# Performance work log

Hardware: AMD Instinct MI355X
Metric: run time of the kernel (lower is better)

Reference implementation:

```python
import jax, jax.numpy as jnp
import numpy as np

FORGET_BIAS = 1.0

def _lstm_cell(x, h, c, W, b):
    # BasicLSTMCell: z = [x, h] @ W + b, gates in (i, j, f, o) order
    z = jnp.concatenate([x, h], axis=-1) @ W + b
    i, j, f, o = jnp.split(z, 4, axis=-1)
    c_new = c * jax.nn.sigmoid(f + FORGET_BIAS) + jax.nn.sigmoid(i) * jnp.tanh(j)
    h_new = jnp.tanh(c_new) * jax.nn.sigmoid(o)
    return h_new, c_new

def setup_inputs() -> dict:
    key = jax.random.key(0)
    k1, k2, k3, k4, k5, k6 = jax.random.split(key, 6)
    B, T, D = 256, 200, 512
    rnn_input = jax.random.normal(k1, (B, T, D), dtype=jnp.float32)
    seq_len = jax.random.randint(k2, (B,), 0, T, dtype=jnp.int32)
    s = 0.05
    W0 = jax.random.normal(k3, (2 * D, 4 * D), dtype=jnp.float32) * s
    b0 = jax.random.normal(k4, (4 * D,), dtype=jnp.float32) * s
    W1 = jax.random.normal(k5, (2 * D, 4 * D), dtype=jnp.float32) * s
    b1 = jax.random.normal(k6, (4 * D,), dtype=jnp.float32) * s
    return {"rnn_input": rnn_input, "seq_len": seq_len, "W0": W0, "b0": b0, "W1": W1, "b1": b1}

def reference(rnn_input, seq_len, W0, b0, W1, b1):
    B, T, D = rnn_input.shape
    h0 = jnp.zeros((B, D), rnn_input.dtype)
    init = (h0, h0, h0, h0)  # (h_l0, c_l0, h_l1, c_l1)

    def step(carry, inp):
        h0, c0, h1, c1 = carry
        x_t, t = inp
        # layer 0 (plain LSTM)
        h0n, c0n = _lstm_cell(x_t, h0, c0, W0, b0)
        # layer 1 (ResidualWrapper: out = cell_out + input)
        h1n, c1n = _lstm_cell(h0n, h1, c1, W1, b1)
        y = h1n + h0n
        # dynamic_rnn semantics: past seq_len, output zero and state copy-through
        valid = (t < seq_len)[:, None]
        h0n = jnp.where(valid, h0n, h0)
        c0n = jnp.where(valid, c0n, c0)
        h1n = jnp.where(valid, h1n, h1)
        c1n = jnp.where(valid, c1n, c1)
        y = jnp.where(valid, y, 0.0)
        return (h0n, c0n, h1n, c1n), y

    xs = (jnp.swapaxes(rnn_input, 0, 1), jnp.arange(T, dtype=seq_len.dtype))
    _, ys = jax.lax.scan(step, init, xs)  # ys: [T, B, D]
    return jnp.swapaxes(ys, 0, 1)  # [B, T, D]
```

## Files before the change

kernel.cpp:

```cpp
#include <hip/hip_runtime.h>

using short8 = __attribute__((ext_vector_type(8))) short;
using f32x4  = __attribute__((ext_vector_type(4))) float;
typedef unsigned short u16;
typedef unsigned int   u32;
typedef unsigned long long u64;

constexpr int Bn = 256;
constexpr int Tn = 200;
constexpr int Dn = 512;

__device__ __forceinline__ u16 f2bf(float x) {
  union { float f; unsigned u; } v; v.f = x;
  unsigned r = v.u + 0x7FFFu + ((v.u >> 16) & 1u);
  return (u16)(r >> 16);
}
__device__ __forceinline__ float sigm(float x) { return 1.0f / (1.0f + __expf(-x)); }
__device__ __forceinline__ float tanhe(float x) { return 1.0f - 2.0f / (__expf(2.0f * x) + 1.0f); }

__global__ void cvt_x_frag(const float* __restrict__ x, u16* __restrict__ xf) {
  int i = blockIdx.x * 256 + threadIdx.x;
  int lane = i & 63;
  int kkd  = (i >> 6) & 15;
  int rf   = (i >> 10) & 3;
  int mt_t = i >> 12;
  int t = mt_t % 200, mtile = mt_t / 200;
  int row = mtile * 64 + rf * 16 + (lane & 15);
  int k0  = kkd * 32 + (lane >> 4) * 8;
  const float* s = x + ((size_t)row * Tn + t) * Dn + k0;
  float4 v0 = *reinterpret_cast<const float4*>(s);
  float4 v1 = *reinterpret_cast<const float4*>(s + 4);
  short8 r;
  r[0]=(short)f2bf(v0.x); r[1]=(short)f2bf(v0.y); r[2]=(short)f2bf(v0.z); r[3]=(short)f2bf(v0.w);
  r[4]=(short)f2bf(v1.x); r[5]=(short)f2bf(v1.y); r[6]=(short)f2bf(v1.z); r[7]=(short)f2bf(v1.w);
  reinterpret_cast<short8*>(xf)[i] = r;
}

__global__ void cvt_w_frag(const float* __restrict__ W0, const float* __restrict__ W1,
                           u16* __restrict__ Wf) {
  __shared__ u16 T[64][65];
  int b = blockIdx.x;
  int nt = b & 31, kt = (b >> 5) & 15, role = b >> 9;
  const float* W = role ? W1 : W0;
  int t = threadIdx.x;
  int k0 = kt * 64, n0 = nt * 64;
  int kr = t >> 6, nl = t & 63;
#pragma unroll
  for (int r = 0; r < 16; ++r) {
    int k = r * 4 + kr;
    T[k][nl] = f2bf(W[(size_t)(k0 + k) * 2048 + n0 + nl]);
  }
  __syncthreads();
  int g = n0 >> 9;
  int dslBase = (n0 & 511) >> 4;
  int kkBase  = k0 >> 5;
  int lane = t & 63, grp = t >> 6;
  int lr = lane & 15, lk = lane >> 4;
#pragma unroll
  for (int c = grp; c < 8; c += 4) {
    int dslL = c & 3, kkL = c >> 2;
    int dsl = dslBase + dslL, kk = kkBase + kkL;
    short8 v;
#pragma unroll
    for (int e = 0; e < 8; ++e)
      v[e] = (short)T[kkL * 32 + lk * 8 + e][dslL * 16 + lr];
    *reinterpret_cast<short8*>(Wf + ((((size_t)(role * 32 + dsl) * 4 + g) * 32 + kk) * 64 + lane) * 8) = v;
  }
}

#define MFMA16 __builtin_amdgcn_mfma_f32_16x16x32_bf16
#define GLOAD_LDS(g, l) __builtin_amdgcn_global_load_lds(                    \
    (const __attribute__((address_space(1))) void*)(g),                      \
    (__attribute__((address_space(3))) void*)(l), 16, 0, 0)

#define ISS4C(A0, A1, A2, A3, P)                                             \
  asm volatile("global_load_dwordx4 %0, %4, off sc0 sc1\n\t"                 \
               "global_load_dwordx4 %1, %4, off offset:1024 sc0 sc1\n\t"     \
               "global_load_dwordx4 %2, %4, off offset:2048 sc0 sc1\n\t"     \
               "global_load_dwordx4 %3, %4, off offset:3072 sc0 sc1"         \
               : "=v"(A0), "=v"(A1), "=v"(A2), "=v"(A3) : "v"(P) : "memory")
#define ISS4N(A0, A1, A2, A3, P)                                             \
  asm volatile("global_load_dwordx4 %0, %4, off\n\t"                         \
               "global_load_dwordx4 %1, %4, off offset:1024\n\t"             \
               "global_load_dwordx4 %2, %4, off offset:2048\n\t"             \
               "global_load_dwordx4 %3, %4, off offset:3072"                 \
               : "=v"(A0), "=v"(A1), "=v"(A2), "=v"(A3) : "v"(P) : "memory")
#define WAITV(N)                                                             \
  asm volatile("s_waitcnt vmcnt(" #N ")" ::: "memory");                      \
  __builtin_amdgcn_sched_barrier(0)
#define MMK(av, kk) {                                                        \
    short8 w0 = *reinterpret_cast<const short8*>(WL + (kk) * 1024);          \
    short8 w1 = *reinterpret_cast<const short8*>(WL + 32768 + (kk) * 1024);  \
    short8 w2 = *reinterpret_cast<const short8*>(WL + 65536 + (kk) * 1024);  \
    short8 w3 = *reinterpret_cast<const short8*>(WL + 98304 + (kk) * 1024);  \
    ac0 = MFMA16(av, w0, ac0, 0, 0, 0);                                      \
    ac1 = MFMA16(av, w1, ac1, 0, 0, 0);                                      \
    ac2 = MFMA16(av, w2, ac2, 0, 0, 0);                                      \
    ac3 = MFMA16(av, w3, ac3, 0, 0, 0); }

extern "C" __global__ void __launch_bounds__(256, 1)
rnn_persist(const u16* __restrict__ xf, const u16* __restrict__ Wf,
            const float* __restrict__ b0, const float* __restrict__ b1,
            const int* __restrict__ seq,
            u16* __restrict__ hf0, u16* __restrict__ hf1,
            u32* __restrict__ bar, float* __restrict__ out) {
  extern __shared__ __align__(16) char smem[];
  const int blk = blockIdx.x;
  const int q = blk & 7;
  const int role = q & 1;
  const int mtile = q >> 1;
  const int dsl = blk >> 3;
  const int tid = threadIdx.x;
  const int rf = tid >> 6, lane = tid & 63;

  {
    const char* gsrc = reinterpret_cast<const char*>(Wf)
                     + (size_t)(role * 32 + dsl) * 131072 + tid * 16;
    char* lds = smem + tid * 16;
#pragma unroll
    for (int i = 0; i < 32; ++i)
      GLOAD_LDS(gsrc + i * 4096, lds + i * 4096);
  }

  const char* xfb = reinterpret_cast<const char*>(xf);
  const char* h0b = reinterpret_cast<const char*>(hf0);
  const char* h1b = reinterpret_cast<const char*>(hf1);
  const int aoff = rf * 16384 + lane * 16;
  const char* WL = smem + lane * 16;

  const int d0 = dsl * 16 + (lane & 15);
  const float* bias = role ? b1 : b0;
  const float bg0 = bias[d0], bg1 = bias[512 + d0], bg2 = bias[1024 + d0], bg3 = bias[1536 + d0];
  const int rowB = mtile * 64 + rf * 16 + (lane >> 4) * 4;
  int sl[4];
#pragma unroll
  for (int e = 0; e < 4; ++e) sl[e] = seq[rowB + e];

  const int kkd = dsl >> 1;
  const int lane_t_base = ((((dsl & 1) << 1) | ((lane & 15) >> 3)) << 4) + (lane >> 4) * 4;
  const size_t hoff0 = (size_t)mtile * 32768 + (size_t)(rf * 16 + kkd) * 512
                     + (size_t)lane_t_base * 8 + (lane & 7);

  u16* hfSelf = role ? hf1 : hf0;
  u16* stg = reinterpret_cast<u16*>(smem + 131072);
  const int uu = tid & 63;
  const size_t o8 = (size_t)((mtile * 4 + rf) * 16 + kkd) * 128
                  + ((dsl & 1) * 32 + (uu >> 1)) * 2 + (uu & 1);
  u32* flagme = bar + mtile * 64 + role * 32 + dsl;
  const u32* fb = bar + mtile * 64 + tid;

  float creg[4]  = {0.f, 0.f, 0.f, 0.f};
  float hkeep[4] = {0.f, 0.f, 0.f, 0.f};

  __syncthreads();

#pragma unroll 1
  for (int p = 0; p <= Tn; ++p) {
    const bool act = role ? (p >= 1) : (p < Tn);
    const int Rp = (p & 1) ^ 1, Wp = p & 1;
    if (act) {
      const int tcur = role ? (p - 1) : p;
      const size_t hRp = (size_t)Rp * 262144 + (size_t)mtile * 65536;
      const char* Alo = (role == 0)
          ? xfb + ((size_t)mtile * Tn + p) * 65536 + aoff
          : h0b + hRp + aoff;
      const char* Ahi = (role == 0) ? h0b + hRp + aoff : h1b + hRp + aoff;

      const char* hra = reinterpret_cast<const char*>(
          reinterpret_cast<const u16*>(h0b) + (size_t)Rp * 131072 + hoff0);
      u32 hn0, hn1, hn2, hn3;
      asm volatile("global_load_ushort %0, %4, off sc0 sc1\n\t"
                   "global_load_ushort %1, %4, off offset:16 sc0 sc1\n\t"
                   "global_load_ushort %2, %4, off offset:32 sc0 sc1\n\t"
                   "global_load_ushort %3, %4, off offset:48 sc0 sc1"
                   : "=v"(hn0), "=v"(hn1), "=v"(hn2), "=v"(hn3) : "v"(hra) : "memory");

      short8 A0,A1,A2,A3,A4,A5,A6,A7,A8,A9,A10,A11,A12,A13,A14,A15;
      short8 B0,B1,B2,B3,B4,B5,B6,B7,B8,B9,B10,B11,B12,B13,B14,B15;
      if (role == 0) {
        ISS4N(A0,A1,A2,A3,    Alo);
        ISS4N(A4,A5,A6,A7,    Alo + 4096);
        ISS4N(A8,A9,A10,A11,  Alo + 8192);
        ISS4N(A12,A13,A14,A15,Alo + 12288);
      } else {
        ISS4C(A0,A1,A2,A3,    Alo);
        ISS4C(A4,A5,A6,A7,    Alo + 4096);
        ISS4C(A8,A9,A10,A11,  Alo + 8192);
        ISS4C(A12,A13,A14,A15,Alo + 12288);
      }
      ISS4C(B0,B1,B2,B3,    Ahi);
      ISS4C(B4,B5,B6,B7,    Ahi + 4096);
      ISS4C(B8,B9,B10,B11,  Ahi + 8192);
      ISS4C(B12,B13,B14,B15,Ahi + 12288);

      f32x4 ac0 = {0.f,0.f,0.f,0.f}, ac1 = {0.f,0.f,0.f,0.f};
      f32x4 ac2 = {0.f,0.f,0.f,0.f}, ac3 = {0.f,0.f,0.f,0.f};

      WAITV(28); MMK(A0,0)  MMK(A1,1)  MMK(A2,2)  MMK(A3,3)
      WAITV(24); MMK(A4,4)  MMK(A5,5)  MMK(A6,6)  MMK(A7,7)
      WAITV(20); MMK(A8,8)  MMK(A9,9)  MMK(A10,10) MMK(A11,11)
      WAITV(16); MMK(A12,12) MMK(A13,13) MMK(A14,14) MMK(A15,15)
      WAITV(12); MMK(B0,16) MMK(B1,17) MMK(B2,18) MMK(B3,19)
      WAITV(8);  MMK(B4,20) MMK(B5,21) MMK(B6,22) MMK(B7,23)
      WAITV(4);  MMK(B8,24) MMK(B9,25) MMK(B10,26) MMK(B11,27)
      WAITV(0);  MMK(B12,28) MMK(B13,29) MMK(B14,30) MMK(B15,31)

      const u32 hnv[4] = {hn0, hn1, hn2, hn3};
#pragma unroll
      for (int e = 0; e < 4; ++e) {
        float zi = ac0[e] + bg0, zj = ac1[e] + bg1, zf = ac2[e] + bg2, zo = ac3[e] + bg3;
        float cprev = creg[e];
        float cn = cprev * sigm(zf + 1.0f) + sigm(zi) * tanhe(zj);
        float hn = tanhe(cn) * sigm(zo);
        bool valid = tcur < sl[e];
        float hk = valid ? hn : hkeep[e];
        creg[e] = valid ? cn : cprev;
        hkeep[e] = hk;
        stg[rf * 256 + (((lane & 15) >> 3) * 16 + (lane >> 4) * 4 + e) * 8 + (lane & 7)] = f2bf(hk);
        if (role) {
          union { float f; u32 u; } hv; hv.u = hnv[e] << 16;
          out[((size_t)(rowB + e) * Tn + tcur) * Dn + d0] = valid ? (hn + hv.f) : 0.0f;
        }
      }
      __syncthreads();
      {
        u64 v = reinterpret_cast<const u64*>(stg)[tid];
        u64* ha = reinterpret_cast<u64*>(hfSelf + (size_t)Wp * 131072) + o8;
        asm volatile("global_store_dwordx2 %0, %1, off sc0 sc1" :: "v"(ha), "v"(v) : "memory");
      }
      asm volatile("s_waitcnt vmcnt(0)" ::: "memory");
    }

    if (p == Tn) break;

    __syncthreads();
    if (tid == 0) {
      u32 tv = (u32)(p + 1);
      asm volatile("global_store_dword %0, %1, off sc0 sc1" :: "v"(flagme), "v"(tv) : "memory");
    }
    if (tid < 64) {
      const int tgt = p + 1;
      u32 fv;
      do {
        asm volatile("global_load_dword %0, %1, off sc0 sc1\n\t"
                     "s_waitcnt vmcnt(0)"
                     : "=v"(fv) : "v"(fb) : "memory");
      } while (!__all((int)fv >= tgt));
    }
    __syncthreads();
  }
}

#define LDA(kk) (*reinterpret_cast<const short8*>(                           \
    (kk) < 16 ? (Alo + (size_t)(kk) * 1024) : (Ahi + (size_t)((kk) - 16) * 1024)))

extern "C" __global__ void __launch_bounds__(256, 1)
rnn_step(const u16* __restrict__ xf, const u16* __restrict__ Wf,
         const float* __restrict__ b0, const float* __restrict__ b1,
         const int* __restrict__ seq,
         u16* __restrict__ hf0, u16* __restrict__ hf1,
         float* __restrict__ cbuf, float* __restrict__ out, int p) {
  extern __shared__ __align__(16) char smem[];
  const int blk = blockIdx.x;
  const int role = blk & 1;
  const int mtile = (blk >> 1) & 3;
  const int dsl = blk >> 3;
  const bool act = role ? (p >= 1) : (p < Tn);
  if (!act) return;

  const int tid = threadIdx.x;
  const int rf = tid >> 6, lane = tid & 63;
  const int Rp = (p & 1) ^ 1, Wp = p & 1;
  const int tcur = role ? (p - 1) : p;

  {
    const char* gsrc = reinterpret_cast<const char*>(Wf)
                     + (size_t)(role * 32 + dsl) * 131072 + tid * 16;
    char* lds = smem + tid * 16;
#pragma unroll
    for (int i = 0; i < 32; ++i)
      GLOAD_LDS(gsrc + i * 4096, lds + i * 4096);
  }

  const char* h0base = reinterpret_cast<const char*>(hf0);
  const char* h1base = reinterpret_cast<const char*>(hf1);
  const size_t hRp = (size_t)Rp * 262144 + (size_t)mtile * 65536;
  const int aoff = rf * 16384 + lane * 16;

  const char* Alo;
  const char* Ahi;
  if (role == 0) {
    Alo = reinterpret_cast<const char*>(xf) + ((size_t)mtile * Tn + p) * 65536 + aoff;
    Ahi = h0base + hRp + aoff;
  } else {
    Alo = h0base + hRp + aoff;
    Ahi = h1base + hRp + aoff;
  }
  const char* WL = smem + lane * 16;

  short8 ca0 = LDA(0), ca1 = LDA(1), ca2 = LDA(2), ca3 = LDA(3);

  const int d0 = dsl * 16 + (lane & 15);
  const float* bias = role ? b1 : b0;
  const float bg0 = bias[d0], bg1 = bias[512 + d0], bg2 = bias[1024 + d0], bg3 = bias[1536 + d0];
  const int rowB = mtile * 64 + rf * 16 + (lane >> 4) * 4;
  int sl[4];
#pragma unroll
  for (int e = 0; e < 4; ++e) sl[e] = seq[rowB + e];

  const int kkd = dsl >> 1;
  const int lane_t_base = ((((dsl & 1) << 1) | ((lane & 15) >> 3)) << 4) + (lane >> 4) * 4;
  const size_t hoff0 = (size_t)mtile * 32768 + (size_t)(rf * 16 + kkd) * 512
                     + (size_t)lane_t_base * 8 + (lane & 7);

  u16 h0nraw[4];
  if (role) {
    const u16* hr = reinterpret_cast<const u16*>(h0base) + (size_t)Rp * 131072;
#pragma unroll
    for (int e = 0; e < 4; ++e) h0nraw[e] = hr[hoff0 + e * 8];
  }
  float* cme = cbuf + ((size_t)blk * 256 + tid) * 4;
  float cpre[4];
#pragma unroll
  for (int e = 0; e < 4; ++e) cpre[e] = cme[e];
  u16* hfSelf = role ? hf1 : hf0;
  const u16* hprev = hfSelf + (size_t)Rp * 131072;
  u16 hp16[4];
#pragma unroll
  for (int e = 0; e < 4; ++e) hp16[e] = hprev[hoff0 + e * 8];

  __syncthreads();

  f32x4 ac0 = {0.f,0.f,0.f,0.f}, ac1 = {0.f,0.f,0.f,0.f};
  f32x4 ac2 = {0.f,0.f,0.f,0.f}, ac3 = {0.f,0.f,0.f,0.f};
  short8 na0, na1, na2, na3;
#pragma unroll
  for (int c = 0; c < 8; ++c) {
    const int k0 = c * 4;
    if (c < 7) {
      na0 = LDA(k0 + 4); na1 = LDA(k0 + 5); na2 = LDA(k0 + 6); na3 = LDA(k0 + 7);
    }
#pragma unroll
    for (int j = 0; j < 4; ++j) {
      const int kk = k0 + j;
      short8 a = (j == 0) ? ca0 : (j == 1) ? ca1 : (j == 2) ? ca2 : ca3;
      short8 w0 = *reinterpret_cast<const short8*>(WL + kk * 1024);
      short8 w1 = *reinterpret_cast<const short8*>(WL + 32768 + kk * 1024);
      short8 w2 = *reinterpret_cast<const short8*>(WL + 65536 + kk * 1024);
      short8 w3 = *reinterpret_cast<const short8*>(WL + 98304 + kk * 1024);
      ac0 = MFMA16(a, w0, ac0, 0, 0, 0);
      ac1 = MFMA16(a, w1, ac1, 0, 0, 0);
      ac2 = MFMA16(a, w2, ac2, 0, 0, 0);
      ac3 = MFMA16(a, w3, ac3, 0, 0, 0);
    }
    ca0 = na0; ca1 = na1; ca2 = na2; ca3 = na3;
  }

  u16* stg = reinterpret_cast<u16*>(smem + 131072);
#pragma unroll
  for (int e = 0; e < 4; ++e) {
    float zi = ac0[e] + bg0, zj = ac1[e] + bg1, zf = ac2[e] + bg2, zo = ac3[e] + bg3;
    float cprev = cpre[e];
    float cn = cprev * sigm(zf + 1.0f) + sigm(zi) * tanhe(zj);
    float hn = tanhe(cn) * sigm(zo);
    bool valid = tcur < sl[e];
    union { float f; u32 u; } hp; hp.u = ((u32)hp16[e]) << 16;
    float hkeep = valid ? hn : hp.f;
    cme[e] = valid ? cn : cprev;
    stg[rf * 256 + (((lane & 15) >> 3) * 16 + (lane >> 4) * 4 + e) * 8 + (lane & 7)] = f2bf(hkeep);
    if (role) {
      union { float f; u32 u; } hv; hv.u = ((u32)h0nraw[e]) << 16;
      out[((size_t)(rowB + e) * Tn + tcur) * Dn + d0] = valid ? (hn + hv.f) : 0.0f;
    }
  }
  __syncthreads();
  {
    const int rft = tid >> 6, u = tid & 63;
    u64 v = reinterpret_cast<const u64*>(stg)[tid];
    u64* hw8 = reinterpret_cast<u64*>(hfSelf + (size_t)Wp * 131072);
    size_t o8 = (size_t)((mtile * 4 + rft) * 16 + kkd) * 128 + ((dsl & 1) * 32 + (u >> 1)) * 2 + (u & 1);
    hw8[o8] = v;
  }
}

extern "C" void kernel_launch(void* const* d_in, const int* in_sizes, int n_in,
                              void* d_out, int out_size, void* d_ws, size_t ws_size,
                              hipStream_t stream) {
  (void)in_sizes; (void)n_in; (void)out_size; (void)ws_size;
  const float* x  = (const float*)d_in[0];
  const int* seq  = (const int*)d_in[1];
  const float* W0 = (const float*)d_in[2];
  const float* b0 = (const float*)d_in[3];
  const float* W1 = (const float*)d_in[4];
  const float* b1 = (const float*)d_in[5];
  float* out = (float*)d_out;

  char* ws = (char*)d_ws;
  u16*  xf   = (u16*)(ws);
  u16*  Wf   = (u16*)(ws + 52428800);
  u16*  hf0  = (u16*)(ws + 60817408);
  u16*  hf1  = (u16*)(ws + 61341696);
  u32*  bar  = (u32*)(ws + 61865984);
  float* cbuf = (float*)(ws + 61865984);

  hipMemsetAsync(ws + 60817408, 0, 2097152, stream);
  hipLaunchKernelGGL(cvt_x_frag, dim3(12800), dim3(256), 0, stream, x, xf);
  hipLaunchKernelGGL(cvt_w_frag, dim3(1024), dim3(256), 0, stream, W0, W1, Wf);

  hipFuncSetAttribute((const void*)rnn_persist,
                      hipFuncAttributeMaxDynamicSharedMemorySize, 133120);
  hipFuncSetAttribute((const void*)rnn_step,
                      hipFuncAttributeMaxDynamicSharedMemorySize, 133120);

  void* args[] = { (void*)&xf, (void*)&Wf, (void*)&b0, (void*)&b1, (void*)&seq,
                   (void*)&hf0, (void*)&hf1, (void*)&bar, (void*)&out };
  hipError_t err = hipLaunchCooperativeKernel((void*)rnn_persist, dim3(256), dim3(256),
                                              args, 133120, stream);
  if (err != hipSuccess) {
    for (int p = 0; p <= Tn; ++p) {
      hipLaunchKernelGGL(rnn_step, dim3(256), dim3(256), 133120, stream,
                         xf, Wf, b0, b1, seq, hf0, hf1, cbuf, out, p);
    }
  }
}
```

Before: 1.203 ms.

## Prefetch next-step x tiles and defer output stores past the barrier

Layer-0 blocks now issue the input x fragment loads for step p+1 before the inter-block barrier, so that load latency overlaps the spin-wait instead of sitting on the recurrent critical path. Layer-1 blocks buffer their outputs in registers and write them after signalling the flag, which keeps the output stores off the pre-barrier vmcnt(0) wait. Memory clobbers are dropped from the load asm and the sched_barrier mask is relaxed to give the compiler more scheduling freedom. The risks are higher register pressure from the 16 prefetch registers held live across the loop, and possible ordering hazards from removing the memory clobbers.

```diff
diff --git a/kernel.cpp b/kernel.cpp
--- a/kernel.cpp
+++ b/kernel.cpp
@@ -78,16 +78,16 @@
                "global_load_dwordx4 %1, %4, off offset:1024 sc0 sc1\n\t"     \
                "global_load_dwordx4 %2, %4, off offset:2048 sc0 sc1\n\t"     \
                "global_load_dwordx4 %3, %4, off offset:3072 sc0 sc1"         \
-               : "=v"(A0), "=v"(A1), "=v"(A2), "=v"(A3) : "v"(P) : "memory")
+               : "=v"(A0), "=v"(A1), "=v"(A2), "=v"(A3) : "v"(P))
 #define ISS4N(A0, A1, A2, A3, P)                                             \
   asm volatile("global_load_dwordx4 %0, %4, off\n\t"                         \
                "global_load_dwordx4 %1, %4, off offset:1024\n\t"             \
                "global_load_dwordx4 %2, %4, off offset:2048\n\t"             \
                "global_load_dwordx4 %3, %4, off offset:3072"                 \
-               : "=v"(A0), "=v"(A1), "=v"(A2), "=v"(A3) : "v"(P) : "memory")
+               : "=v"(A0), "=v"(A1), "=v"(A2), "=v"(A3) : "v"(P))
 #define WAITV(N)                                                             \
-  asm volatile("s_waitcnt vmcnt(" #N ")" ::: "memory");                      \
-  __builtin_amdgcn_sched_barrier(0)
+  asm volatile("s_waitcnt vmcnt(" #N ")");                                   \
+  __builtin_amdgcn_sched_barrier(0x3F7)
 #define MMK(av, kk) {                                                        \
     short8 w0 = *reinterpret_cast<const short8*>(WL + (kk) * 1024);          \
     short8 w1 = *reinterpret_cast<const short8*>(WL + 32768 + (kk) * 1024);  \
@@ -152,58 +152,74 @@
   float creg[4]  = {0.f, 0.f, 0.f, 0.f};
   float hkeep[4] = {0.f, 0.f, 0.f, 0.f};
 
+  short8 A0,A1,A2,A3,A4,A5,A6,A7,A8,A9,A10,A11,A12,A13,A14,A15;
+  short8 B0,B1,B2,B3,B4,B5,B6,B7,B8,B9,B10,B11,B12,B13,B14,B15;
+
+  if (role == 0) {
+    const char* An = xfb + ((size_t)mtile * Tn + 0) * 65536 + aoff;
+    ISS4N(A0,A1,A2,A3,    An);
+    ISS4N(A4,A5,A6,A7,    An + 4096);
+    ISS4N(A8,A9,A10,A11,  An + 8192);
+    ISS4N(A12,A13,A14,A15,An + 12288);
+  }
+
   __syncthreads();
 
 #pragma unroll 1
   for (int p = 0; p <= Tn; ++p) {
     const bool act = role ? (p >= 1) : (p < Tn);
     const int Rp = (p & 1) ^ 1, Wp = p & 1;
+    float outv[4] = {0.f, 0.f, 0.f, 0.f};
     if (act) {
       const int tcur = role ? (p - 1) : p;
       const size_t hRp = (size_t)Rp * 262144 + (size_t)mtile * 65536;
-      const char* Alo = (role == 0)
-          ? xfb + ((size_t)mtile * Tn + p) * 65536 + aoff
-          : h0b + hRp + aoff;
-      const char* Ahi = (role == 0) ? h0b + hRp + aoff : h1b + hRp + aoff;
-
-      const char* hra = reinterpret_cast<const char*>(
-          reinterpret_cast<const u16*>(h0b) + (size_t)Rp * 131072 + hoff0);
-      u32 hn0, hn1, hn2, hn3;
-      asm volatile("global_load_ushort %0, %4, off sc0 sc1\n\t"
-                   "global_load_ushort %1, %4, off offset:16 sc0 sc1\n\t"
-                   "global_load_ushort %2, %4, off offset:32 sc0 sc1\n\t"
-                   "global_load_ushort %3, %4, off offset:48 sc0 sc1"
-                   : "=v"(hn0), "=v"(hn1), "=v"(hn2), "=v"(hn3) : "v"(hra) : "memory");
-
-      short8 A0,A1,A2,A3,A4,A5,A6,A7,A8,A9,A10,A11,A12,A13,A14,A15;
-      short8 B0,B1,B2,B3,B4,B5,B6,B7,B8,B9,B10,B11,B12,B13,B14,B15;
+
+      f32x4 ac0 = {0.f,0.f,0.f,0.f}, ac1 = {0.f,0.f,0.f,0.f};
+      f32x4 ac2 = {0.f,0.f,0.f,0.f}, ac3 = {0.f,0.f,0.f,0.f};
+      u32 hn0 = 0, hn1 = 0, hn2 = 0, hn3 = 0;
+
       if (role == 0) {
-        ISS4N(A0,A1,A2,A3,    Alo);
-        ISS4N(A4,A5,A6,A7,    Alo + 4096);
-        ISS4N(A8,A9,A10,A11,  Alo + 8192);
-        ISS4N(A12,A13,A14,A15,Alo + 12288);
+        const char* Bh = h0b + hRp + aoff;
+        ISS4C(B0,B1,B2,B3,    Bh);
+        ISS4C(B4,B5,B6,B7,    Bh + 4096);
+        ISS4C(B8,B9,B10,B11,  Bh + 8192);
+        ISS4C(B12,B13,B14,B15,Bh + 12288);
+        WAITV(16);
+        MMK(A0,0)  MMK(A1,1)  MMK(A2,2)  MMK(A3,3)
+        MMK(A4,4)  MMK(A5,5)  MMK(A6,6)  MMK(A7,7)
+        MMK(A8,8)  MMK(A9,9)  MMK(A10,10) MMK(A11,11)
+        MMK(A12,12) MMK(A13,13) MMK(A14,14) MMK(A15,15)
+        WAITV(12); MMK(B0,16) MMK(B1,17) MMK(B2,18) MMK(B3,19)
+        WAITV(8);  MMK(B4,20) MMK(B5,21) MMK(B6,22) MMK(B7,23)
+        WAITV(4);  MMK(B8,24) MMK(B9,25) MMK(B10,26) MMK(B11,27)
+        WAITV(0);  MMK(B12,28) MMK(B13,29) MMK(B14,30) MMK(B15,31)
       } else {
+        const char* hra = reinterpret_cast<const char*>(
+            reinterpret_cast<const u16*>(h0b) + (size_t)Rp * 131072 + hoff0);
+        asm volatile("global_load_ushort %0, %4, off sc0 sc1\n\t"
+                     "global_load_ushort %1, %4, off offset:16 sc0 sc1\n\t"
+                     "global_load_ushort %2, %4, off offset:32 sc0 sc1\n\t"
+                     "global_load_ushort %3, %4, off offset:48 sc0 sc1"
+                     : "=v"(hn0), "=v"(hn1), "=v"(hn2), "=v"(hn3) : "v"(hra));
+        const char* Alo = h0b + hRp + aoff;
+        const char* Ahi = h1b + hRp + aoff;
         ISS4C(A0,A1,A2,A3,    Alo);
         ISS4C(A4,A5,A6,A7,    Alo + 4096);
         ISS4C(A8,A9,A10,A11,  Alo + 8192);
         ISS4C(A12,A13,A14,A15,Alo + 12288);
+        ISS4C(B0,B1,B2,B3,    Ahi);
+        ISS4C(B4,B5,B6,B7,    Ahi + 4096);
+        ISS4C(B8,B9,B10,B11,  Ahi + 8192);
+        ISS4C(B12,B13,B14,B15,Ahi + 12288);
+        WAITV(28); MMK(A0,0)  MMK(A1,1)  MMK(A2,2)  MMK(A3,3)
+        WAITV(24); MMK(A4,4)  MMK(A5,5)  MMK(A6,6)  MMK(A7,7)
+        WAITV(20); MMK(A8,8)  MMK(A9,9)  MMK(A10,10) MMK(A11,11)
+        WAITV(16); MMK(A12,12) MMK(A13,13) MMK(A14,14) MMK(A15,15)
+        WAITV(12); MMK(B0,16) MMK(B1,17) MMK(B2,18) MMK(B3,19)
+        WAITV(8);  MMK(B4,20) MMK(B5,21) MMK(B6,22) MMK(B7,23)
+        WAITV(4);  MMK(B8,24) MMK(B9,25) MMK(B10,26) MMK(B11,27)
+        WAITV(0);  MMK(B12,28) MMK(B13,29) MMK(B14,30) MMK(B15,31)
       }
-      ISS4C(B0,B1,B2,B3,    Ahi);
-      ISS4C(B4,B5,B6,B7,    Ahi + 4096);
-      ISS4C(B8,B9,B10,B11,  Ahi + 8192);
-      ISS4C(B12,B13,B14,B15,Ahi + 12288);
-
-      f32x4 ac0 = {0.f,0.f,0.f,0.f}, ac1 = {0.f,0.f,0.f,0.f};
-      f32x4 ac2 = {0.f,0.f,0.f,0.f}, ac3 = {0.f,0.f,0.f,0.f};
-
-      WAITV(28); MMK(A0,0)  MMK(A1,1)  MMK(A2,2)  MMK(A3,3)
-      WAITV(24); MMK(A4,4)  MMK(A5,5)  MMK(A6,6)  MMK(A7,7)
-      WAITV(20); MMK(A8,8)  MMK(A9,9)  MMK(A10,10) MMK(A11,11)
-      WAITV(16); MMK(A12,12) MMK(A13,13) MMK(A14,14) MMK(A15,15)
-      WAITV(12); MMK(B0,16) MMK(B1,17) MMK(B2,18) MMK(B3,19)
-      WAITV(8);  MMK(B4,20) MMK(B5,21) MMK(B6,22) MMK(B7,23)
-      WAITV(4);  MMK(B8,24) MMK(B9,25) MMK(B10,26) MMK(B11,27)
-      WAITV(0);  MMK(B12,28) MMK(B13,29) MMK(B14,30) MMK(B15,31)
 
       const u32 hnv[4] = {hn0, hn1, hn2, hn3};
 #pragma unroll
@@ -219,7 +235,7 @@
         stg[rf * 256 + (((lane & 15) >> 3) * 16 + (lane >> 4) * 4 + e) * 8 + (lane & 7)] = f2bf(hk);
         if (role) {
           union { float f; u32 u; } hv; hv.u = hnv[e] << 16;
-          out[((size_t)(rowB + e) * Tn + tcur) * Dn + d0] = valid ? (hn + hv.f) : 0.0f;
+          outv[e] = valid ? (hn + hv.f) : 0.0f;
         }
       }
       __syncthreads();
@@ -231,12 +247,32 @@
       asm volatile("s_waitcnt vmcnt(0)" ::: "memory");
     }
 
-    if (p == Tn) break;
+    if (p == Tn) {
+      if (role) {
+#pragma unroll
+        for (int e = 0; e < 4; ++e)
+          out[((size_t)(rowB + e) * Tn + (Tn - 1)) * Dn + d0] = outv[e];
+      }
+      break;
+    }
+
+    if (role == 0 && p + 1 < Tn) {
+      const char* An = xfb + ((size_t)mtile * Tn + (p + 1)) * 65536 + aoff;
+      ISS4N(A0,A1,A2,A3,    An);
+      ISS4N(A4,A5,A6,A7,    An + 4096);
+      ISS4N(A8,A9,A10,A11,  An + 8192);
+      ISS4N(A12,A13,A14,A15,An + 12288);
+    }
 
     __syncthreads();
     if (tid == 0) {
       u32 tv = (u32)(p + 1);
       asm volatile("global_store_dword %0, %1, off sc0 sc1" :: "v"(flagme), "v"(tv) : "memory");
+    }
+    if (role && p >= 1) {
+#pragma unroll
+      for (int e = 0; e < 4; ++e)
+        out[((size_t)(rowB + e) * Tn + (p - 1)) * Dn + d0] = outv[e];
     }
     if (tid < 64) {
       const int tgt = p + 1;
```

Result: slower. 1.582 ms (+31.5%).

## Use 2-wave blocks with two row tiles per wave sharing LDS weight reads

Applied to the files above, without the earlier changes.

The persistent kernel now runs 128 threads per block, and each wave computes two 16-row M tiles. Every weight fragment read from LDS therefore feeds two MFMAs, halving LDS weight traffic per MFMA. A-operand loads are rotated through a 4-slot register ring so the second-half loads overlap the first-half MFMAs. The output stores are deferred until after the flag publish, so they overlap the barrier poll, and memory clobbers are relaxed to give the scheduler more freedom. The cost is higher register pressure and fewer waves per CU to hide latency.

```diff
diff --git a/kernel.cpp b/kernel.cpp
--- a/kernel.cpp
+++ b/kernel.cpp
@@ -78,16 +78,223 @@
                "global_load_dwordx4 %1, %4, off offset:1024 sc0 sc1\n\t"     \
                "global_load_dwordx4 %2, %4, off offset:2048 sc0 sc1\n\t"     \
                "global_load_dwordx4 %3, %4, off offset:3072 sc0 sc1"         \
-               : "=v"(A0), "=v"(A1), "=v"(A2), "=v"(A3) : "v"(P) : "memory")
+               : "=v"(A0), "=v"(A1), "=v"(A2), "=v"(A3) : "v"(P))
 #define ISS4N(A0, A1, A2, A3, P)                                             \
   asm volatile("global_load_dwordx4 %0, %4, off\n\t"                         \
                "global_load_dwordx4 %1, %4, off offset:1024\n\t"             \
                "global_load_dwordx4 %2, %4, off offset:2048\n\t"             \
                "global_load_dwordx4 %3, %4, off offset:3072"                 \
-               : "=v"(A0), "=v"(A1), "=v"(A2), "=v"(A3) : "v"(P) : "memory")
+               : "=v"(A0), "=v"(A1), "=v"(A2), "=v"(A3) : "v"(P))
 #define WAITV(N)                                                             \
-  asm volatile("s_waitcnt vmcnt(" #N ")" ::: "memory");                      \
-  __builtin_amdgcn_sched_barrier(0)
+  asm volatile("s_waitcnt vmcnt(" #N ")");                                   \
+  __builtin_amdgcn_sched_barrier(0x3F7)
+#define MMK2(alo, ahi, kk) {                                                 \
+    short8 w0 = *reinterpret_cast<const short8*>(WL + (kk) * 1024);          \
+    short8 w1 = *reinterpret_cast<const short8*>(WL + 32768 + (kk) * 1024);  \
+    short8 w2 = *reinterpret_cast<const short8*>(WL + 65536 + (kk) * 1024);  \
+    short8 w3 = *reinterpret_cast<const short8*>(WL + 98304 + (kk) * 1024);  \
+    pa0 = MFMA16(alo, w0, pa0, 0, 0, 0); qa0 = MFMA16(ahi, w0, qa0, 0, 0, 0);\
+    pa1 = MFMA16(alo, w1, pa1, 0, 0, 0); qa1 = MFMA16(ahi, w1, qa1, 0, 0, 0);\
+    pa2 = MFMA16(alo, w2, pa2, 0, 0, 0); qa2 = MFMA16(ahi, w2, qa2, 0, 0, 0);\
+    pa3 = MFMA16(alo, w3, pa3, 0, 0, 0); qa3 = MFMA16(ahi, w3, qa3, 0, 0, 0); }
+#define ISSN_SLOT(S, P) ISS4N(S##a0,S##a1,S##a2,S##a3,(P));                  \
+                        ISS4N(S##b0,S##b1,S##b2,S##b3,(P)+16384);
+#define ISSC_SLOT(S, P) ISS4C(S##a0,S##a1,S##a2,S##a3,(P));                  \
+                        ISS4C(S##b0,S##b1,S##b2,S##b3,(P)+16384);
+#define CONS_SLOT(S, KK) MMK2(S##a0,S##b0,(KK))   MMK2(S##a1,S##b1,(KK)+1)   \
+                         MMK2(S##a2,S##b2,(KK)+2) MMK2(S##a3,S##b3,(KK)+3)
+#define POLL(tgtexpr) {                                                      \
+    const int tgt_ = (tgtexpr); u32 fv_;                                     \
+    do {                                                                     \
+      asm volatile("global_load_dword %0, %1, off sc0 sc1\n\t"               \
+                   "s_waitcnt vmcnt(0)" : "=v"(fv_) : "v"(fbw) : "memory");  \
+    } while (!__all((int)fv_ >= tgt_));                                      \
+  }
+#define FLAG(val) {                                                          \
+    u32 tv_ = (u32)(val);                                                    \
+    asm volatile("global_store_dword %0, %1, off sc0 sc1" :: "v"(flagme), "v"(tv_) : "memory"); }
+
+extern "C" __global__ void __launch_bounds__(128, 1)
+rnn_persist(const u16* __restrict__ xf, const u16* __restrict__ Wf,
+            const float* __restrict__ b0, const float* __restrict__ b1,
+            const int* __restrict__ seq,
+            u16* __restrict__ hf0, u16* __restrict__ hf1,
+            u32* __restrict__ bar, float* __restrict__ out) {
+  extern __shared__ __align__(16) char smem[];
+  const int blk = blockIdx.x;
+  const int role = blk & 1;
+  const int mtile = (blk >> 1) & 3;
+  const int dsl = blk >> 3;
+  const int tid = threadIdx.x;
+  const int wid = tid >> 6, lane = tid & 63;
+  const int rlo = wid * 2;
+
+  {
+    const char* gsrc = reinterpret_cast<const char*>(Wf)
+                     + (size_t)(role * 32 + dsl) * 131072 + tid * 16;
+    char* lds = smem + tid * 16;
+#pragma unroll
+    for (int i = 0; i < 64; ++i)
+      GLOAD_LDS(gsrc + i * 2048, lds + i * 2048);
+  }
+
+  const char* xfb = reinterpret_cast<const char*>(xf);
+  const char* h0b = reinterpret_cast<const char*>(hf0);
+  const char* h1b = reinterpret_cast<const char*>(hf1);
+  const char* WL = smem + lane * 16;
+
+  const int d0 = dsl * 16 + (lane & 15);
+  const float* bias = role ? b1 : b0;
+  const float bg0 = bias[d0], bg1 = bias[512 + d0], bg2 = bias[1024 + d0], bg3 = bias[1536 + d0];
+  const int rowB0 = mtile * 64 + rlo * 16 + (lane >> 4) * 4;
+  const int rowB1 = rowB0 + 16;
+  int sl0[4], sl1[4];
+#pragma unroll
+  for (int e = 0; e < 4; ++e) { sl0[e] = seq[rowB0 + e]; sl1[e] = seq[rowB1 + e]; }
+
+  const int kkd = dsl >> 1;
+  const int lane_t_base = ((((dsl & 1) << 1) | ((lane & 15) >> 3)) << 4) + (lane >> 4) * 4;
+  const size_t hoffA = (size_t)mtile * 32768 + (size_t)(rlo * 16 + kkd) * 512
+                     + (size_t)lane_t_base * 8 + (lane & 7);
+
+  u16* stg = reinterpret_cast<u16*>(smem + 131072);
+  const size_t o8A = (size_t)((mtile * 4 + rlo) * 16 + kkd) * 128
+                   + ((dsl & 1) * 32 + (lane >> 1)) * 2 + (lane & 1);
+  const size_t o8B = o8A + 2048;
+  u32* flagme = bar + mtile * 64 + role * 32 + dsl;
+  const u32* fbw = bar + mtile * 64 + lane;
+
+  float creg0[4] = {0.f,0.f,0.f,0.f}, creg1[4] = {0.f,0.f,0.f,0.f};
+  float hk0[4]   = {0.f,0.f,0.f,0.f}, hk1[4]   = {0.f,0.f,0.f,0.f};
+  const f32x4 z4 = {0.f, 0.f, 0.f, 0.f};
+
+  __syncthreads();
+
+#pragma unroll 1
+  for (int p = 0; p <= Tn; ++p) {
+    const int Rp = (p & 1) ^ 1, Wp = p & 1;
+    float ov0[4] = {0.f,0.f,0.f,0.f}, ov1[4] = {0.f,0.f,0.f,0.f};
+    const bool act = role ? (p >= 1) : (p < Tn);
+    if (act) {
+      const int tcur = role ? (p - 1) : p;
+      const size_t hRp = (size_t)Rp * 262144 + (size_t)mtile * 65536;
+      f32x4 pa0 = z4, pa1 = z4, pa2 = z4, pa3 = z4;
+      f32x4 qa0 = z4, qa1 = z4, qa2 = z4, qa3 = z4;
+      u32 hA0=0,hA1=0,hA2=0,hA3=0, hB0=0,hB1=0,hB2=0,hB3=0;
+      short8 s0a0,s0a1,s0a2,s0a3,s0b0,s0b1,s0b2,s0b3;
+      short8 s1a0,s1a1,s1a2,s1a3,s1b0,s1b1,s1b2,s1b3;
+      short8 s2a0,s2a1,s2a2,s2a3,s2b0,s2b1,s2b2,s2b3;
+      short8 s3a0,s3a1,s3a2,s3a3,s3b0,s3b1,s3b2,s3b3;
+
+      if (role == 0) {
+        const char* AX = xfb + ((size_t)mtile * Tn + p) * 65536 + rlo * 16384 + lane * 16;
+        const char* AH = h0b + hRp + rlo * 16384 + lane * 16;
+        ISSN_SLOT(s0, AX);         ISSN_SLOT(s1, AX + 4096);
+        ISSN_SLOT(s2, AX + 8192);  ISSN_SLOT(s3, AX + 12288);
+        WAITV(24); CONS_SLOT(s0, 0);  ISSC_SLOT(s0, AH);
+        WAITV(24); CONS_SLOT(s1, 4);  ISSC_SLOT(s1, AH + 4096);
+        WAITV(24); CONS_SLOT(s2, 8);  ISSC_SLOT(s2, AH + 8192);
+        WAITV(24); CONS_SLOT(s3, 12); ISSC_SLOT(s3, AH + 12288);
+        WAITV(24); CONS_SLOT(s0, 16);
+        WAITV(16); CONS_SLOT(s1, 20);
+        WAITV(8);  CONS_SLOT(s2, 24);
+        WAITV(0);  CONS_SLOT(s3, 28);
+      } else {
+        const char* hraA = h0b + (size_t)Rp * 262144 + hoffA * 2;
+        const char* hraB = hraA + 16384;
+        asm volatile("global_load_ushort %0, %4, off sc0 sc1\n\t"
+                     "global_load_ushort %1, %4, off offset:16 sc0 sc1\n\t"
+                     "global_load_ushort %2, %4, off offset:32 sc0 sc1\n\t"
+                     "global_load_ushort %3, %4, off offset:48 sc0 sc1"
+                     : "=v"(hA0), "=v"(hA1), "=v"(hA2), "=v"(hA3) : "v"(hraA));
+        asm volatile("global_load_ushort %0, %4, off sc0 sc1\n\t"
+                     "global_load_ushort %1, %4, off offset:16 sc0 sc1\n\t"
+                     "global_load_ushort %2, %4, off offset:32 sc0 sc1\n\t"
+                     "global_load_ushort %3, %4, off offset:48 sc0 sc1"
+                     : "=v"(hB0), "=v"(hB1), "=v"(hB2), "=v"(hB3) : "v"(hraB));
+        const char* AA = h0b + hRp + rlo * 16384 + lane * 16;
+        const char* AB = h1b + hRp + rlo * 16384 + lane * 16;
+        ISSC_SLOT(s0, AA);         ISSC_SLOT(s1, AA + 4096);
+        ISSC_SLOT(s2, AA + 8192);  ISSC_SLOT(s3, AA + 12288);
+        WAITV(24); CONS_SLOT(s0, 0);  ISSC_SLOT(s0, AB);
+        WAITV(24); CONS_SLOT(s1, 4);  ISSC_SLOT(s1, AB + 4096);
+        WAITV(24); CONS_SLOT(s2, 8);  ISSC_SLOT(s2, AB + 8192);
+        WAITV(24); CONS_SLOT(s3, 12); ISSC_SLOT(s3, AB + 12288);
+        WAITV(24); CONS_SLOT(s0, 16);
+        WAITV(16); CONS_SLOT(s1, 20);
+        WAITV(8);  CONS_SLOT(s2, 24);
+        WAITV(0);  CONS_SLOT(s3, 28);
+      }
+
+      const u32 hAv[4] = {hA0, hA1, hA2, hA3};
+      const u32 hBv[4] = {hB0, hB1, hB2, hB3};
+#pragma unroll
+      for (int e = 0; e < 4; ++e) {
+        {
+          float zi = pa0[e] + bg0, zj = pa1[e] + bg1, zf = pa2[e] + bg2, zo = pa3[e] + bg3;
+          float cp = creg0[e];
+          float cn = cp * sigm(zf + 1.0f) + sigm(zi) * tanhe(zj);
+          float hn = tanhe(cn) * sigm(zo);
+          bool valid = tcur < sl0[e];
+          float hk = valid ? hn : hk0[e];
+          creg0[e] = valid ? cn : cp;
+          hk0[e] = hk;
+          stg[rlo * 256 + (((lane & 15) >> 3) * 16 + (lane >> 4) * 4 + e) * 8 + (lane & 7)] = f2bf(hk);
+          if (role) { union { float f; u32 u; } hv; hv.u = hAv[e] << 16;
+                      ov0[e] = valid ? (hn + hv.f) : 0.0f; }
+        }
+        {
+          float zi = qa0[e] + bg0, zj = qa1[e] + bg1, zf = qa2[e] + bg2, zo = qa3[e] + bg3;
+          float cp = creg1[e];
+          float cn = cp * sigm(zf + 1.0f) + sigm(zi) * tanhe(zj);
+          float hn = tanhe(cn) * sigm(zo);
+          bool valid = tcur < sl1[e];
+          float hk = valid ? hn : hk1[e];
+          creg1[e] = valid ? cn : cp;
+          hk1[e] = hk;
+          stg[(rlo + 1) * 256 + (((lane & 15) >> 3) * 16 + (lane >> 4) * 4 + e) * 8 + (lane & 7)] = f2bf(hk);
+          if (role) { union { float f; u32 u; } hv; hv.u = hBv[e] << 16;
+                      ov1[e] = valid ? (hn + hv.f) : 0.0f; }
+        }
+      }
+      if (!role || p < Tn) {
+        asm volatile("s_waitcnt lgkmcnt(0)" ::: "memory");
+        u16* hw = (role ? hf1 : hf0) + (size_t)Wp * 131072;
+        u64 v0 = reinterpret_cast<const u64*>(stg)[rlo * 64 + lane];
+        u64 v1 = reinterpret_cast<const u64*>(stg)[(rlo + 1) * 64 + lane];
+        u64* haA = reinterpret_cast<u64*>(hw) + o8A;
+        u64* haB = reinterpret_cast<u64*>(hw) + o8B;
+        asm volatile("global_store_dwordx2 %0, %1, off sc0 sc1" :: "v"(haA), "v"(v0) : "memory");
+        asm volatile("global_store_dwordx2 %0, %1, off sc0 sc1" :: "v"(haB), "v"(v1) : "memory");
+        asm volatile("s_waitcnt vmcnt(0)" ::: "memory");
+      }
+    }
+
+    if (p == Tn) {
+      if (role) {
+#pragma unroll
+        for (int e = 0; e < 4; ++e) {
+          out[((size_t)(rowB0 + e) * Tn + (Tn - 1)) * Dn + d0] = ov0[e];
+          out[((size_t)(rowB1 + e) * Tn + (Tn - 1)) * Dn + d0] = ov1[e];
+        }
+      }
+      break;
+    }
+
+    __builtin_amdgcn_s_barrier();
+    if (tid == 0) FLAG(p + 1);
+    if (role && p >= 1) {
+#pragma unroll
+      for (int e = 0; e < 4; ++e) {
+        out[((size_t)(rowB0 + e) * Tn + (p - 1)) * Dn + d0] = ov0[e];
+        out[((size_t)(rowB1 + e) * Tn + (p - 1)) * Dn + d0] = ov1[e];
+      }
+    }
+    if (tid < 64) POLL(p + 1);
+    __builtin_amdgcn_s_barrier();
+  }
+}
+
 #define MMK(av, kk) {                                                        \
     short8 w0 = *reinterpret_cast<const short8*>(WL + (kk) * 1024);          \
     short8 w1 = *reinterpret_cast<const short8*>(WL + 32768 + (kk) * 1024);  \
@@ -97,160 +304,6 @@
     ac1 = MFMA16(av, w1, ac1, 0, 0, 0);                                      \
     ac2 = MFMA16(av, w2, ac2, 0, 0, 0);                                      \
     ac3 = MFMA16(av, w3, ac3, 0, 0, 0); }
-
-extern "C" __global__ void __launch_bounds__(256, 1)
-rnn_persist(const u16* __restrict__ xf, const u16* __restrict__ Wf,
-            const float* __restrict__ b0, const float* __restrict__ b1,
-            const int* __restrict__ seq,
-            u16* __restrict__ hf0, u16* __restrict__ hf1,
-            u32* __restrict__ bar, float* __restrict__ out) {
-  extern __shared__ __align__(16) char smem[];
-  const int blk = blockIdx.x;
-  const int q = blk & 7;
-  const int role = q & 1;
-  const int mtile = q >> 1;
-  const int dsl = blk >> 3;
-  const int tid = threadIdx.x;
-  const int rf = tid >> 6, lane = tid & 63;
-
-  {
-    const char* gsrc = reinterpret_cast<const char*>(Wf)
-                     + (size_t)(role * 32 + dsl) * 131072 + tid * 16;
-    char* lds = smem + tid * 16;
-#pragma unroll
-    for (int i = 0; i < 32; ++i)
-      GLOAD_LDS(gsrc + i * 4096, lds + i * 4096);
-  }
-
-  const char* xfb = reinterpret_cast<const char*>(xf);
-  const char* h0b = reinterpret_cast<const char*>(hf0);
-  const char* h1b = reinterpret_cast<const char*>(hf1);
-  const int aoff = rf * 16384 + lane * 16;
-  const char* WL = smem + lane * 16;
-
-  const int d0 = dsl * 16 + (lane & 15);
-  const float* bias = role ? b1 : b0;
-  const float bg0 = bias[d0], bg1 = bias[512 + d0], bg2 = bias[1024 + d0], bg3 = bias[1536 + d0];
-  const int rowB = mtile * 64 + rf * 16 + (lane >> 4) * 4;
-  int sl[4];
-#pragma unroll
-  for (int e = 0; e < 4; ++e) sl[e] = seq[rowB + e];
-
-  const int kkd = dsl >> 1;
-  const int lane_t_base = ((((dsl & 1) << 1) | ((lane & 15) >> 3)) << 4) + (lane >> 4) * 4;
-  const size_t hoff0 = (size_t)mtile * 32768 + (size_t)(rf * 16 + kkd) * 512
-                     + (size_t)lane_t_base * 8 + (lane & 7);
-
-  u16* hfSelf = role ? hf1 : hf0;
-  u16* stg = reinterpret_cast<u16*>(smem + 131072);
-  const int uu = tid & 63;
-  const size_t o8 = (size_t)((mtile * 4 + rf) * 16 + kkd) * 128
-                  + ((dsl & 1) * 32 + (uu >> 1)) * 2 + (uu & 1);
-  u32* flagme = bar + mtile * 64 + role * 32 + dsl;
-  const u32* fb = bar + mtile * 64 + tid;
-
-  float creg[4]  = {0.f, 0.f, 0.f, 0.f};
-  float hkeep[4] = {0.f, 0.f, 0.f, 0.f};
-
-  __syncthreads();
-
-#pragma unroll 1
-  for (int p = 0; p <= Tn; ++p) {
-    const bool act = role ? (p >= 1) : (p < Tn);
-    const int Rp = (p & 1) ^ 1, Wp = p & 1;
-    if (act) {
-      const int tcur = role ? (p - 1) : p;
-      const size_t hRp = (size_t)Rp * 262144 + (size_t)mtile * 65536;
-      const char* Alo = (role == 0)
-          ? xfb + ((size_t)mtile * Tn + p) * 65536 + aoff
-          : h0b + hRp + aoff;
-      const char* Ahi = (role == 0) ? h0b + hRp + aoff : h1b + hRp + aoff;
-
-      const char* hra = reinterpret_cast<const char*>(
-          reinterpret_cast<const u16*>(h0b) + (size_t)Rp * 131072 + hoff0);
-      u32 hn0, hn1, hn2, hn3;
-      asm volatile("global_load_ushort %0, %4, off sc0 sc1\n\t"
-                   "global_load_ushort %1, %4, off offset:16 sc0 sc1\n\t"
-                   "global_load_ushort %2, %4, off offset:32 sc0 sc1\n\t"
-                   "global_load_ushort %3, %4, off offset:48 sc0 sc1"
-                   : "=v"(hn0), "=v"(hn1), "=v"(hn2), "=v"(hn3) : "v"(hra) : "memory");
-
-      short8 A0,A1,A2,A3,A4,A5,A6,A7,A8,A9,A10,A11,A12,A13,A14,A15;
-      short8 B0,B1,B2,B3,B4,B5,B6,B7,B8,B9,B10,B11,B12,B13,B14,B15;
-      if (role == 0) {
-        ISS4N(A0,A1,A2,A3,    Alo);
-        ISS4N(A4,A5,A6,A7,    Alo + 4096);
-        ISS4N(A8,A9,A10,A11,  Alo + 8192);
-        ISS4N(A12,A13,A14,A15,Alo + 12288);
-      } else {
-        ISS4C(A0,A1,A2,A3,    Alo);
-        ISS4C(A4,A5,A6,A7,    Alo + 4096);
-        ISS4C(A8,A9,A10,A11,  Alo + 8192);
-        ISS4C(A12,A13,A14,A15,Alo + 12288);
-      }
-      ISS4C(B0,B1,B2,B3,    Ahi);
-      ISS4C(B4,B5,B6,B7,    Ahi + 4096);
-      ISS4C(B8,B9,B10,B11,  Ahi + 8192);
-      ISS4C(B12,B13,B14,B15,Ahi + 12288);
-
-      f32x4 ac0 = {0.f,0.f,0.f,0.f}, ac1 = {0.f,0.f,0.f,0.f};
-      f32x4 ac2 = {0.f,0.f,0.f,0.f}, ac3 = {0.f,0.f,0.f,0.f};
-
-      WAITV(28); MMK(A0,0)  MMK(A1,1)  MMK(A2,2)  MMK(A3,3)
-      WAITV(24); MMK(A4,4)  MMK(A5,5)  MMK(A6,6)  MMK(A7,7)
-      WAITV(20); MMK(A8,8)  MMK(A9,9)  MMK(A10,10) MMK(A11,11)
-      WAITV(16); MMK(A12,12) MMK(A13,13) MMK(A14,14) MMK(A15,15)
-      WAITV(12); MMK(B0,16) MMK(B1,17) MMK(B2,18) MMK(B3,19)
-      WAITV(8);  MMK(B4,20) MMK(B5,21) MMK(B6,22) MMK(B7,23)
-      WAITV(4);  MMK(B8,24) MMK(B9,25) MMK(B10,26) MMK(B11,27)
-      WAITV(0);  MMK(B12,28) MMK(B13,29) MMK(B14,30) MMK(B15,31)
-
-      const u32 hnv[4] = {hn0, hn1, hn2, hn3};
-#pragma unroll
-      for (int e = 0; e < 4; ++e) {
-        float zi = ac0[e] + bg0, zj = ac1[e] + bg1, zf = ac2[e] + bg2, zo = ac3[e] + bg3;
-        float cprev = creg[e];
-        float cn = cprev * sigm(zf + 1.0f) + sigm(zi) * tanhe(zj);
-        float hn = tanhe(cn) * sigm(zo);
-        bool valid = tcur < sl[e];
-        float hk = valid ? hn : hkeep[e];
-        creg[e] = valid ? cn : cprev;
-        hkeep[e] = hk;
-        stg[rf * 256 + (((lane & 15) >> 3) * 16 + (lane >> 4) * 4 + e) * 8 + (lane & 7)] = f2bf(hk);
-        if (role) {
-          union { float f; u32 u; } hv; hv.u = hnv[e] << 16;
-          out[((size_t)(rowB + e) * Tn + tcur) * Dn + d0] = valid ? (hn + hv.f) : 0.0f;
-        }
-      }
-      __syncthreads();
-      {
-        u64 v = reinterpret_cast<const u64*>(stg)[tid];
-        u64* ha = reinterpret_cast<u64*>(hfSelf + (size_t)Wp * 131072) + o8;
-        asm volatile("global_store_dwordx2 %0, %1, off sc0 sc1" :: "v"(ha), "v"(v) : "memory");
-      }
-      asm volatile("s_waitcnt vmcnt(0)" ::: "memory");
-    }
-
-    if (p == Tn) break;
-
-    __syncthreads();
-    if (tid == 0) {
-      u32 tv = (u32)(p + 1);
-      asm volatile("global_store_dword %0, %1, off sc0 sc1" :: "v"(flagme), "v"(tv) : "memory");
-    }
-    if (tid < 64) {
-      const int tgt = p + 1;
-      u32 fv;
-      do {
-        asm volatile("global_load_dword %0, %1, off sc0 sc1\n\t"
-                     "s_waitcnt vmcnt(0)"
-                     : "=v"(fv) : "v"(fb) : "memory");
-      } while (!__all((int)fv >= tgt));
-    }
-    __syncthreads();
-  }
-}
-
 #define LDA(kk) (*reinterpret_cast<const short8*>(                           \
     (kk) < 16 ? (Alo + (size_t)(kk) * 1024) : (Ahi + (size_t)((kk) - 16) * 1024)))
 
@@ -344,14 +397,7 @@
     for (int j = 0; j < 4; ++j) {
       const int kk = k0 + j;
       short8 a = (j == 0) ? ca0 : (j == 1) ? ca1 : (j == 2) ? ca2 : ca3;
-      short8 w0 = *reinterpret_cast<const short8*>(WL + kk * 1024);
-      short8 w1 = *reinterpret_cast<const short8*>(WL + 32768 + kk * 1024);
-      short8 w2 = *reinterpret_cast<const short8*>(WL + 65536 + kk * 1024);
-      short8 w3 = *reinterpret_cast<const short8*>(WL + 98304 + kk * 1024);
-      ac0 = MFMA16(a, w0, ac0, 0, 0, 0);
-      ac1 = MFMA16(a, w1, ac1, 0, 0, 0);
-      ac2 = MFMA16(a, w2, ac2, 0, 0, 0);
-      ac3 = MFMA16(a, w3, ac3, 0, 0, 0);
+      MMK(a, kk)
     }
     ca0 = na0; ca1 = na1; ca2 = na2; ca3 = na3;
   }
@@ -414,7 +460,7 @@
 
   void* args[] = { (void*)&xf, (void*)&Wf, (void*)&b0, (void*)&b1, (void*)&seq,
                    (void*)&hf0, (void*)&hf1, (void*)&bar, (void*)&out };
-  hipError_t err = hipLaunchCooperativeKernel((void*)rnn_persist, dim3(256), dim3(256),
+  hipError_t err = hipLaunchCooperativeKernel((void*)rnn_persist, dim3(256), dim3(128),
                                               args, 133120, stream);
   if (err != hipSuccess) {
     for (int p = 0; p <= Tn; ++p) {
```

Measured after the change: 1.826 ms. 51.8% more time.

## Trim barriers and defer output stores off the recurrent critical path

Applied to the files above, without the earlier changes.

The block-wide __syncthreads before the h-staging readback becomes a wave-local lgkmcnt wait, since each wave reads back only the staging bytes it wrote. The loop barriers become bare s_barrier without the implicit fences. Output stores are buffered in registers and issued after the step flag is published, so global writes of y no longer delay the cross-block handoff. Dropping the memory clobbers on the inline load asm gives the compiler more scheduling freedom, at the risk of subtle ordering issues with the cross-block h buffers.

```diff
diff --git a/kernel.cpp b/kernel.cpp
--- a/kernel.cpp
+++ b/kernel.cpp
@@ -78,13 +78,13 @@
                "global_load_dwordx4 %1, %4, off offset:1024 sc0 sc1\n\t"     \
                "global_load_dwordx4 %2, %4, off offset:2048 sc0 sc1\n\t"     \
                "global_load_dwordx4 %3, %4, off offset:3072 sc0 sc1"         \
-               : "=v"(A0), "=v"(A1), "=v"(A2), "=v"(A3) : "v"(P) : "memory")
+               : "=v"(A0), "=v"(A1), "=v"(A2), "=v"(A3) : "v"(P))
 #define ISS4N(A0, A1, A2, A3, P)                                             \
   asm volatile("global_load_dwordx4 %0, %4, off\n\t"                         \
                "global_load_dwordx4 %1, %4, off offset:1024\n\t"             \
                "global_load_dwordx4 %2, %4, off offset:2048\n\t"             \
                "global_load_dwordx4 %3, %4, off offset:3072"                 \
-               : "=v"(A0), "=v"(A1), "=v"(A2), "=v"(A3) : "v"(P) : "memory")
+               : "=v"(A0), "=v"(A1), "=v"(A2), "=v"(A3) : "v"(P))
 #define WAITV(N)                                                             \
   asm volatile("s_waitcnt vmcnt(" #N ")" ::: "memory");                      \
   __builtin_amdgcn_sched_barrier(0)
@@ -143,9 +143,8 @@
 
   u16* hfSelf = role ? hf1 : hf0;
   u16* stg = reinterpret_cast<u16*>(smem + 131072);
-  const int uu = tid & 63;
   const size_t o8 = (size_t)((mtile * 4 + rf) * 16 + kkd) * 128
-                  + ((dsl & 1) * 32 + (uu >> 1)) * 2 + (uu & 1);
+                  + ((dsl & 1) * 32 + (lane >> 1)) * 2 + (lane & 1);
   u32* flagme = bar + mtile * 64 + role * 32 + dsl;
   const u32* fb = bar + mtile * 64 + tid;
 
@@ -158,6 +157,7 @@
   for (int p = 0; p <= Tn; ++p) {
     const bool act = role ? (p >= 1) : (p < Tn);
     const int Rp = (p & 1) ^ 1, Wp = p & 1;
+    float outv[4] = {0.f, 0.f, 0.f, 0.f};
     if (act) {
       const int tcur = role ? (p - 1) : p;
       const size_t hRp = (size_t)Rp * 262144 + (size_t)mtile * 65536;
@@ -173,7 +173,7 @@
                    "global_load_ushort %1, %4, off offset:16 sc0 sc1\n\t"
                    "global_load_ushort %2, %4, off offset:32 sc0 sc1\n\t"
                    "global_load_ushort %3, %4, off offset:48 sc0 sc1"
-                   : "=v"(hn0), "=v"(hn1), "=v"(hn2), "=v"(hn3) : "v"(hra) : "memory");
+                   : "=v"(hn0), "=v"(hn1), "=v"(hn2), "=v"(hn3) : "v"(hra));
 
       short8 A0,A1,A2,A3,A4,A5,A6,A7,A8,A9,A10,A11,A12,A13,A14,A15;
       short8 B0,B1,B2,B3,B4,B5,B6,B7,B8,B9,B10,B11,B12,B13,B14,B15;
@@ -219,10 +219,10 @@
         stg[rf * 256 + (((lane & 15) >> 3) * 16 + (lane >> 4) * 4 + e) * 8 + (lane & 7)] = f2bf(hk);
         if (role) {
           union { float f; u32 u; } hv; hv.u = hnv[e] << 16;
-          out[((size_t)(rowB + e) * Tn + tcur) * Dn + d0] = valid ? (hn + hv.f) : 0.0f;
+          outv[e] = valid ? (hn + hv.f) : 0.0f;
         }
       }
-      __syncthreads();
+      asm volatile("s_waitcnt lgkmcnt(0)" ::: "memory");
       {
         u64 v = reinterpret_cast<const u64*>(stg)[tid];
         u64* ha = reinterpret_cast<u64*>(hfSelf + (size_t)Wp * 131072) + o8;
@@ -231,12 +231,24 @@
       asm volatile("s_waitcnt vmcnt(0)" ::: "memory");
     }
 
-    if (p == Tn) break;
-
-    __syncthreads();
+    if (p == Tn) {
+      if (role) {
+#pragma unroll
+        for (int e = 0; e < 4; ++e)
+          out[((size_t)(rowB + e) * Tn + (Tn - 1)) * Dn + d0] = outv[e];
+      }
+      break;
+    }
+
+    __builtin_amdgcn_s_barrier();
     if (tid == 0) {
       u32 tv = (u32)(p + 1);
       asm volatile("global_store_dword %0, %1, off sc0 sc1" :: "v"(flagme), "v"(tv) : "memory");
+    }
+    if (role && p >= 1) {
+#pragma unroll
+      for (int e = 0; e < 4; ++e)
+        out[((size_t)(rowB + e) * Tn + (p - 1)) * Dn + d0] = outv[e];
     }
     if (tid < 64) {
       const int tgt = p + 1;
@@ -247,7 +259,7 @@
                      : "=v"(fv) : "v"(fb) : "memory");
       } while (!__all((int)fv >= tgt));
     }
-    __syncthreads();
+    __builtin_amdgcn_s_barrier();
   }
 }
 
```

Measured after the change: 1.273 ms. +5.8%, slower.
